# Optimization experiments

Measured on AMD Instinct MI355X. Metric: run time of the kernel, lower is better.

## Reference

```python
import jax, jax.numpy as jnp
import numpy as np

LOG2 = float(np.log(2.0))

def ssp(x):
    # shifted softplus: softplus(x) - log(2)
    return jax.nn.softplus(x) - LOG2

N_NODES = 50000
N_EDGES = 600000
HID = 128
NF = 128

def setup_inputs() -> dict:
    key = jax.random.key(0)
    ks = jax.random.split(key, 10)
    x = jax.random.normal(ks[0], (N_NODES, HID), dtype=jnp.float32)
    edge_attr = jax.random.normal(ks[1], (N_EDGES, NF), dtype=jnp.float32)
    edge_index = jax.random.randint(ks[2], (2, N_EDGES), 0, N_NODES, dtype=jnp.int32)
    s = 1.0 / np.sqrt(NF)
    fc1_w = jax.random.uniform(ks[3], (NF, HID), jnp.float32, -s, s)   # CFConv.fc1 (no bias)
    f_w1 = jax.random.uniform(ks[4], (NF, NF), jnp.float32, -s, s)     # filter_mlp[0]
    f_b1 = jnp.zeros((NF,), jnp.float32)
    f_w2 = jax.random.uniform(ks[5], (NF, NF), jnp.float32, -s, s)     # filter_mlp[2]
    f_b2 = jnp.zeros((NF,), jnp.float32)
    s_w1 = jax.random.uniform(ks[6], (NF, NF), jnp.float32, -s, s)     # StateMLP.fc1
    s_w2 = jax.random.uniform(ks[7], (NF, NF), jnp.float32, -s, s)     # StateMLP.fc2
    return {"x": x, "edge_attr": edge_attr, "edge_index": edge_index,
            "fc1_w": fc1_w, "f_w1": f_w1, "f_b1": f_b1, "f_w2": f_w2,
            "f_b2": f_b2, "s_w1": s_w1, "s_w2": s_w2}

def reference(x, edge_attr, edge_index, fc1_w, f_w1, f_b1, f_w2, f_b2, s_w1, s_w2):
    src, dst = edge_index[0], edge_index[1]  # x_j = x[src], aggregate at dst
    # filter network on edge attributes: [E, NF]
    W = ssp(ssp(edge_attr @ f_w1.T + f_b1) @ f_w2.T + f_b2)
    # message: gather source nodes, linear transform, filter multiply
    msg = (x[src] @ fc1_w.T) * W                               # [E, NF]
    # scatter-add aggregation into nodes
    agg = jax.ops.segment_sum(msg, dst, num_segments=x.shape[0])  # [N, NF]
    # StateMLP
    return ssp(agg @ s_w1.T) @ s_w2.T
```

## Files before the change

kernel.cpp:

```cpp
#include <hip/hip_runtime.h>

#define F 128

typedef __attribute__((ext_vector_type(8))) __bf16 bf16x8;
typedef __attribute__((ext_vector_type(4))) float floatx4;

__device__ __forceinline__ float ssp(float x) {
    return __logf(fmaf(0.5f, __expf(x), 0.5f));
}

__global__ void prep_kernel(const float* __restrict__ fc1w,
                            const float* __restrict__ fw1,
                            const float* __restrict__ fw2,
                            const float* __restrict__ sw1,
                            const float* __restrict__ sw2,
                            __bf16* __restrict__ fc1h, __bf16* __restrict__ fc1l,
                            __bf16* __restrict__ fw1h, __bf16* __restrict__ fw2h,
                            __bf16* __restrict__ sw1h, __bf16* __restrict__ sw1l,
                            __bf16* __restrict__ sw2h, __bf16* __restrict__ sw2l)
{
    int i = blockIdx.x * blockDim.x + threadIdx.x;
    if (i >= F * F) return;
    float v; __bf16 h;
    v = fc1w[i]; h = (__bf16)v; fc1h[i] = h; fc1l[i] = (__bf16)(v - (float)h);
    v = sw1[i];  h = (__bf16)v; sw1h[i] = h; sw1l[i] = (__bf16)(v - (float)h);
    v = sw2[i];  h = (__bf16)v; sw2h[i] = h; sw2l[i] = (__bf16)(v - (float)h);
    fw1h[i] = (__bf16)fw1[i];
    fw2h[i] = (__bf16)fw2[i];
}

__global__ __launch_bounds__(256) void fc1_kernel(
    const float* __restrict__ x, const __bf16* __restrict__ wh,
    const __bf16* __restrict__ wl, float* __restrict__ y, int M)
{
    const int tid = threadIdx.x;
    const int wv = tid >> 6, lane = tid & 63;
    const int m16 = lane & 15, q = lane >> 4;
    const int g = wv & 1, c = wv >> 1;
    const int rowA0 = blockIdx.x * 32 + g * 16 + m16;
    const int rowA = rowA0 < M ? rowA0 : M - 1;

    floatx4 acc[4] = {};
    #pragma unroll
    for (int ks = 0; ks < 4; ++ks) {
        const int kb = ks * 32 + q * 8;
        const float4* p = (const float4*)(x + (size_t)rowA * F + kb);
        float4 a0 = p[0], a1 = p[1];
        float fv[8] = {a0.x, a0.y, a0.z, a0.w, a1.x, a1.y, a1.z, a1.w};
        bf16x8 ah, al;
        #pragma unroll
        for (int i = 0; i < 8; ++i) {
            __bf16 h = (__bf16)fv[i];
            ah[i] = h; al[i] = (__bf16)(fv[i] - (float)h);
        }
        #pragma unroll
        for (int nt = 0; nt < 4; ++nt) {
            const size_t wo = (size_t)(c * 64 + nt * 16 + m16) * F + kb;
            bf16x8 bh = *(const bf16x8*)(wh + wo);
            bf16x8 bl = *(const bf16x8*)(wl + wo);
            acc[nt] = __builtin_amdgcn_mfma_f32_16x16x32_bf16(ah, bh, acc[nt], 0, 0, 0);
            acc[nt] = __builtin_amdgcn_mfma_f32_16x16x32_bf16(al, bh, acc[nt], 0, 0, 0);
            acc[nt] = __builtin_amdgcn_mfma_f32_16x16x32_bf16(ah, bl, acc[nt], 0, 0, 0);
        }
    }
    const int rowD0 = blockIdx.x * 32 + g * 16 + q * 4;
    #pragma unroll
    for (int nt = 0; nt < 4; ++nt) {
        const int col = c * 64 + nt * 16 + m16;
        #pragma unroll
        for (int r = 0; r < 4; ++r) {
            const int row = rowD0 + r;
            if (row < M) y[(size_t)row * F + col] = acc[nt][r];
        }
    }
}

__global__ __launch_bounds__(256) void edge_kernel(
    const float* __restrict__ edge_attr,
    const int* __restrict__ eidx,
    const float* __restrict__ fb1, const float* __restrict__ fb2,
    const __bf16* __restrict__ fw1, const __bf16* __restrict__ fw2,
    const float* __restrict__ y,
    float* __restrict__ agg, int E)
{
    __shared__ __bf16 h1[64][136];

    const int tid = threadIdx.x;
    const int wv = tid >> 6, lane = tid & 63;
    const int m16 = lane & 15, q = lane >> 4;
    const int e0 = blockIdx.x * 64;
    const int rowA0 = e0 + wv * 16 + m16;
    const int rowA = rowA0 < E ? rowA0 : E - 1;

    floatx4 acc[8] = {};
    #pragma unroll
    for (int ks = 0; ks < 4; ++ks) {
        const int kb = ks * 32 + q * 8;
        const float4* pa = (const float4*)(edge_attr + (size_t)rowA * F + kb);
        float4 a0 = pa[0], a1 = pa[1];
        float fv[8] = {a0.x, a0.y, a0.z, a0.w, a1.x, a1.y, a1.z, a1.w};
        bf16x8 aF;
        #pragma unroll
        for (int i = 0; i < 8; ++i) aF[i] = (__bf16)fv[i];
        #pragma unroll
        for (int nt = 0; nt < 8; ++nt) {
            bf16x8 bF = *(const bf16x8*)(fw1 + (size_t)(nt * 16 + m16) * F + kb);
            acc[nt] = __builtin_amdgcn_mfma_f32_16x16x32_bf16(aF, bF, acc[nt], 0, 0, 0);
        }
    }
    #pragma unroll
    for (int nt = 0; nt < 8; ++nt) {
        const int col = nt * 16 + m16;
        const float b = fb1[col];
        #pragma unroll
        for (int r = 0; r < 4; ++r) {
            const int row = wv * 16 + q * 4 + r;
            h1[row][col] = (__bf16)ssp(acc[nt][r] + b);
        }
    }
    __syncthreads();

    floatx4 zero = {};
    #pragma unroll
    for (int nt = 0; nt < 8; ++nt) acc[nt] = zero;
    #pragma unroll
    for (int ks = 0; ks < 4; ++ks) {
        const int kb = ks * 32 + q * 8;
        bf16x8 aF = *(const bf16x8*)(&h1[wv * 16 + m16][kb]);
        #pragma unroll
        for (int nt = 0; nt < 8; ++nt) {
            bf16x8 bF = *(const bf16x8*)(fw2 + (size_t)(nt * 16 + m16) * F + kb);
            acc[nt] = __builtin_amdgcn_mfma_f32_16x16x32_bf16(aF, bF, acc[nt], 0, 0, 0);
        }
    }

    int src[4], dst[4], ok[4];
    #pragma unroll
    for (int r = 0; r < 4; ++r) {
        const int e = e0 + wv * 16 + q * 4 + r;
        const int ec = e < E ? e : E - 1;
        ok[r] = (e < E);
        src[r] = eidx[ec];
        dst[r] = eidx[E + ec];
    }
    #pragma unroll
    for (int nt = 0; nt < 8; ++nt) {
        const int col = nt * 16 + m16;
        const float b = fb2[col];
        #pragma unroll
        for (int r = 0; r < 4; ++r) {
            if (ok[r]) {
                const float wV = ssp(acc[nt][r] + b);
                const float v = y[(size_t)src[r] * F + col] * wV;
                unsafeAtomicAdd(&agg[(size_t)dst[r] * F + col], v);
            }
        }
    }
}

__global__ __launch_bounds__(256) void state_kernel(
    const float* __restrict__ agg,
    const __bf16* __restrict__ w1h, const __bf16* __restrict__ w1l,
    const __bf16* __restrict__ w2h, const __bf16* __restrict__ w2l,
    float* __restrict__ out, int M)
{
    __shared__ __bf16 hh[32][136];
    __shared__ __bf16 hl[32][136];

    const int tid = threadIdx.x;
    const int wv = tid >> 6, lane = tid & 63;
    const int m16 = lane & 15, q = lane >> 4;
    const int g = wv & 1, c = wv >> 1;
    const int rowA0 = blockIdx.x * 32 + g * 16 + m16;
    const int rowA = rowA0 < M ? rowA0 : M - 1;

    floatx4 acc[4] = {};
    #pragma unroll
    for (int ks = 0; ks < 4; ++ks) {
        const int kb = ks * 32 + q * 8;
        const float4* p = (const float4*)(agg + (size_t)rowA * F + kb);
        float4 a0 = p[0], a1 = p[1];
        float fv[8] = {a0.x, a0.y, a0.z, a0.w, a1.x, a1.y, a1.z, a1.w};
        bf16x8 ah, al;
        #pragma unroll
        for (int i = 0; i < 8; ++i) {
            __bf16 h = (__bf16)fv[i];
            ah[i] = h; al[i] = (__bf16)(fv[i] - (float)h);
        }
        #pragma unroll
        for (int nt = 0; nt < 4; ++nt) {
            const size_t wo = (size_t)(c * 64 + nt * 16 + m16) * F + kb;
            bf16x8 bh = *(const bf16x8*)(w1h + wo);
            bf16x8 bl = *(const bf16x8*)(w1l + wo);
            acc[nt] = __builtin_amdgcn_mfma_f32_16x16x32_bf16(ah, bh, acc[nt], 0, 0, 0);
            acc[nt] = __builtin_amdgcn_mfma_f32_16x16x32_bf16(al, bh, acc[nt], 0, 0, 0);
            acc[nt] = __builtin_amdgcn_mfma_f32_16x16x32_bf16(ah, bl, acc[nt], 0, 0, 0);
        }
    }
    #pragma unroll
    for (int nt = 0; nt < 4; ++nt) {
        const int col = c * 64 + nt * 16 + m16;
        #pragma unroll
        for (int r = 0; r < 4; ++r) {
            const int row = g * 16 + q * 4 + r;
            const float h = ssp(acc[nt][r]);
            const __bf16 H = (__bf16)h;
            hh[row][col] = H;
            hl[row][col] = (__bf16)(h - (float)H);
        }
    }
    __syncthreads();

    floatx4 zero = {};
    #pragma unroll
    for (int nt = 0; nt < 4; ++nt) acc[nt] = zero;
    #pragma unroll
    for (int ks = 0; ks < 4; ++ks) {
        const int kb = ks * 32 + q * 8;
        bf16x8 aH = *(const bf16x8*)(&hh[g * 16 + m16][kb]);
        bf16x8 aL = *(const bf16x8*)(&hl[g * 16 + m16][kb]);
        #pragma unroll
        for (int nt = 0; nt < 4; ++nt) {
            const size_t wo = (size_t)(c * 64 + nt * 16 + m16) * F + kb;
            bf16x8 bh = *(const bf16x8*)(w2h + wo);
            bf16x8 bl = *(const bf16x8*)(w2l + wo);
            acc[nt] = __builtin_amdgcn_mfma_f32_16x16x32_bf16(aH, bh, acc[nt], 0, 0, 0);
            acc[nt] = __builtin_amdgcn_mfma_f32_16x16x32_bf16(aL, bh, acc[nt], 0, 0, 0);
            acc[nt] = __builtin_amdgcn_mfma_f32_16x16x32_bf16(aH, bl, acc[nt], 0, 0, 0);
        }
    }
    const int rowD0 = blockIdx.x * 32 + g * 16 + q * 4;
    #pragma unroll
    for (int nt = 0; nt < 4; ++nt) {
        const int col = c * 64 + nt * 16 + m16;
        #pragma unroll
        for (int r = 0; r < 4; ++r) {
            const int row = rowD0 + r;
            if (row < M) out[(size_t)row * F + col] = acc[nt][r];
        }
    }
}

extern "C" void kernel_launch(void* const* d_in, const int* in_sizes, int n_in,
                              void* d_out, int out_size, void* d_ws, size_t ws_size,
                              hipStream_t stream)
{
    const float* x         = (const float*)d_in[0];
    const float* edge_attr = (const float*)d_in[1];
    const int*   eidx      = (const int*)d_in[2];
    const float* fc1w      = (const float*)d_in[3];
    const float* fw1       = (const float*)d_in[4];
    const float* fb1       = (const float*)d_in[5];
    const float* fw2       = (const float*)d_in[6];
    const float* fb2       = (const float*)d_in[7];
    const float* sw1       = (const float*)d_in[8];
    const float* sw2       = (const float*)d_in[9];
    float* out = (float*)d_out;

    const int N = in_sizes[0] / F;
    const int E = in_sizes[1] / F;

    float* agg = (float*)d_ws;
    float* y   = agg + (size_t)N * F;
    __bf16* wb = (__bf16*)(y + (size_t)N * F);
    const int WSZ = F * F;
    __bf16* fc1h = wb;            __bf16* fc1l = wb + WSZ;
    __bf16* fw1h = wb + 2 * WSZ;  __bf16* fw2h = wb + 3 * WSZ;
    __bf16* sw1h = wb + 4 * WSZ;  __bf16* sw1l = wb + 5 * WSZ;
    __bf16* sw2h = wb + 6 * WSZ;  __bf16* sw2l = wb + 7 * WSZ;

    hipMemsetAsync(agg, 0, (size_t)N * F * sizeof(float), stream);

    prep_kernel<<<(WSZ + 255) / 256, 256, 0, stream>>>(
        fc1w, fw1, fw2, sw1, sw2, fc1h, fc1l, fw1h, fw2h, sw1h, sw1l, sw2h, sw2l);

    fc1_kernel<<<(N + 31) / 32, 256, 0, stream>>>(x, fc1h, fc1l, y, N);

    edge_kernel<<<(E + 63) / 64, 256, 0, stream>>>(
        edge_attr, eidx, fb1, fb2, fw1h, fw2h, y, agg, E);

    state_kernel<<<(N + 31) / 32, 256, 0, stream>>>(
        agg, sw1h, sw1l, sw2h, sw2l, out, N);
}
```

Baseline: 928.0 us.

## Sort edges by destination and combine partial sums before atomic scatter

Adds a histogram, a three-kernel prefix scan and a scatter pass that build a destination-sorted permutation of the edges, along with reordered src/dst arrays. The edge kernel processes edges in sorted order, gathers edge_attr rows through the permutation, and accumulates runs of equal-destination rows in registers before issuing one atomic per run. This is meant to reduce atomic traffic to the aggregation buffer. In exchange it adds several small kernel launches and makes the edge_attr reads indirect, which may hurt their coalescing.

Measured after the change: 1.018 ms. 9.7% more time.

```diff
diff --git a/kernel.cpp b/kernel.cpp
--- a/kernel.cpp
+++ b/kernel.cpp
@@ -29,6 +29,63 @@
     fw2h[i] = (__bf16)fw2[i];
 }
 
+__global__ __launch_bounds__(256) void hist_kernel(const int* __restrict__ eidx,
+                                                   int* __restrict__ cnt, int E)
+{
+    int i = blockIdx.x * 256 + threadIdx.x;
+    if (i < E) atomicAdd(&cnt[eidx[E + i]], 1);
+}
+
+__global__ __launch_bounds__(1024) void scan1_kernel(int* __restrict__ cnt,
+                                                     int* __restrict__ bsums, int N)
+{
+    __shared__ int sd[1024];
+    const int t = threadIdx.x;
+    const int i = blockIdx.x * 1024 + t;
+    int v = (i < N) ? cnt[i] : 0;
+    sd[t] = v;
+    __syncthreads();
+    for (int off = 1; off < 1024; off <<= 1) {
+        int add = (t >= off) ? sd[t - off] : 0;
+        __syncthreads();
+        sd[t] += add;
+        __syncthreads();
+    }
+    if (i < N) cnt[i] = sd[t] - v;
+    if (t == 1023) bsums[blockIdx.x] = sd[t];
+}
+
+__global__ void scan2_kernel(int* __restrict__ bsums, int nb)
+{
+    if (threadIdx.x == 0 && blockIdx.x == 0) {
+        int acc = 0;
+        for (int j = 0; j < nb; ++j) { int c = bsums[j]; bsums[j] = acc; acc += c; }
+    }
+}
+
+__global__ __launch_bounds__(1024) void scan3_kernel(int* __restrict__ cnt,
+                                                     const int* __restrict__ bsums, int N)
+{
+    int i = blockIdx.x * 1024 + threadIdx.x;
+    if (i < N) cnt[i] += bsums[blockIdx.x];
+}
+
+__global__ __launch_bounds__(256) void scatter_kernel(const int* __restrict__ eidx,
+                                                      int* __restrict__ cursor,
+                                                      int* __restrict__ perm,
+                                                      int* __restrict__ ssrc,
+                                                      int* __restrict__ sdst, int E)
+{
+    int i = blockIdx.x * 256 + threadIdx.x;
+    if (i < E) {
+        int d = eidx[E + i];
+        int slot = atomicAdd(&cursor[d], 1);
+        perm[slot] = i;
+        ssrc[slot] = eidx[i];
+        sdst[slot] = d;
+    }
+}
+
 __global__ __launch_bounds__(256) void fc1_kernel(
     const float* __restrict__ x, const __bf16* __restrict__ wh,
     const __bf16* __restrict__ wl, float* __restrict__ y, int M)
@@ -77,7 +134,9 @@
 
 __global__ __launch_bounds__(256) void edge_kernel(
     const float* __restrict__ edge_attr,
-    const int* __restrict__ eidx,
+    const int* __restrict__ perm,
+    const int* __restrict__ ssrc,
+    const int* __restrict__ sdst,
     const float* __restrict__ fb1, const float* __restrict__ fb2,
     const __bf16* __restrict__ fw1, const __bf16* __restrict__ fw2,
     const float* __restrict__ y,
@@ -89,14 +148,15 @@
     const int wv = tid >> 6, lane = tid & 63;
     const int m16 = lane & 15, q = lane >> 4;
     const int e0 = blockIdx.x * 64;
-    const int rowA0 = e0 + wv * 16 + m16;
-    const int rowA = rowA0 < E ? rowA0 : E - 1;
+    const int pA0 = e0 + wv * 16 + m16;
+    const int pA = pA0 < E ? pA0 : E - 1;
+    const int eA = perm[pA];
 
     floatx4 acc[8] = {};
     #pragma unroll
     for (int ks = 0; ks < 4; ++ks) {
         const int kb = ks * 32 + q * 8;
-        const float4* pa = (const float4*)(edge_attr + (size_t)rowA * F + kb);
+        const float4* pa = (const float4*)(edge_attr + (size_t)eA * F + kb);
         float4 a0 = pa[0], a1 = pa[1];
         float fv[8] = {a0.x, a0.y, a0.z, a0.w, a1.x, a1.y, a1.z, a1.w};
         bf16x8 aF;
@@ -137,22 +197,27 @@
     int src[4], dst[4], ok[4];
     #pragma unroll
     for (int r = 0; r < 4; ++r) {
-        const int e = e0 + wv * 16 + q * 4 + r;
-        const int ec = e < E ? e : E - 1;
-        ok[r] = (e < E);
-        src[r] = eidx[ec];
-        dst[r] = eidx[E + ec];
+        const int p = e0 + wv * 16 + q * 4 + r;
+        const int pc = p < E ? p : E - 1;
+        ok[r] = (p < E);
+        src[r] = ssrc[pc];
+        dst[r] = sdst[pc];
     }
     #pragma unroll
     for (int nt = 0; nt < 8; ++nt) {
         const int col = nt * 16 + m16;
         const float b = fb2[col];
+        float run = 0.f;
         #pragma unroll
         for (int r = 0; r < 4; ++r) {
             if (ok[r]) {
                 const float wV = ssp(acc[nt][r] + b);
-                const float v = y[(size_t)src[r] * F + col] * wV;
-                unsafeAtomicAdd(&agg[(size_t)dst[r] * F + col], v);
+                run += y[(size_t)src[r] * F + col] * wV;
+                const bool flush = (r == 3) || (!ok[r + 1]) || (dst[r + 1] != dst[r]);
+                if (flush) {
+                    unsafeAtomicAdd(&agg[(size_t)dst[r] * F + col], run);
+                    run = 0.f;
+                }
             }
         }
     }
@@ -268,16 +333,30 @@
     __bf16* fw1h = wb + 2 * WSZ;  __bf16* fw2h = wb + 3 * WSZ;
     __bf16* sw1h = wb + 4 * WSZ;  __bf16* sw1l = wb + 5 * WSZ;
     __bf16* sw2h = wb + 6 * WSZ;  __bf16* sw2l = wb + 7 * WSZ;
+    int* cnt   = (int*)(wb + 8 * WSZ);
+    int* bsums = cnt + N;
+    int* perm  = bsums + 64;
+    int* ssrc  = perm + E;
+    int* sdst  = ssrc + E;
+
+    const int nb1 = (N + 1023) / 1024;
 
     hipMemsetAsync(agg, 0, (size_t)N * F * sizeof(float), stream);
+    hipMemsetAsync(cnt, 0, (size_t)N * sizeof(int), stream);
 
     prep_kernel<<<(WSZ + 255) / 256, 256, 0, stream>>>(
         fc1w, fw1, fw2, sw1, sw2, fc1h, fc1l, fw1h, fw2h, sw1h, sw1l, sw2h, sw2l);
 
     fc1_kernel<<<(N + 31) / 32, 256, 0, stream>>>(x, fc1h, fc1l, y, N);
 
+    hist_kernel<<<(E + 255) / 256, 256, 0, stream>>>(eidx, cnt, E);
+    scan1_kernel<<<nb1, 1024, 0, stream>>>(cnt, bsums, N);
+    scan2_kernel<<<1, 64, 0, stream>>>(bsums, nb1);
+    scan3_kernel<<<nb1, 1024, 0, stream>>>(cnt, bsums, N);
+    scatter_kernel<<<(E + 255) / 256, 256, 0, stream>>>(eidx, cnt, perm, ssrc, sdst, E);
+
     edge_kernel<<<(E + 63) / 64, 256, 0, stream>>>(
-        edge_attr, eidx, fb1, fb2, fw1h, fw2h, y, agg, E);
+        edge_attr, perm, ssrc, sdst, fb1, fb2, fw1h, fw2h, y, agg, E);
 
     state_kernel<<<(N + 31) / 32, 256, 0, stream>>>(
         agg, sw1h, sw1l, sw2h, sw2l, out, N);
```
